# Optimization experiments

Measured on AMD Instinct MI355X. Metric: run time of the kernel, lower is better.

The kernel has to match this reference:

```python
import jax, jax.numpy as jnp
import numpy as np

B = 2_000_000
ND = 3

def _skew(v):
    # v: [B,3] -> [B,3,3] skew-symmetric matrix
    z = jnp.zeros_like(v[..., 0])
    r0 = jnp.stack([z, -v[..., 2], v[..., 1]], axis=-1)
    r1 = jnp.stack([v[..., 2], z, -v[..., 0]], axis=-1)
    r2 = jnp.stack([-v[..., 1], v[..., 0], z], axis=-1)
    return jnp.stack([r0, r1, r2], axis=-2)

def _rotmat(v):
    # Closed-form expm of skew(v) (Rodrigues). Mathematically identical to tf.linalg.expm.
    th2 = jnp.sum(v * v, axis=-1)                      # [B]
    th = jnp.sqrt(th2)
    small = th < 1e-6
    th_s = jnp.where(small, 1.0, th)
    th2_s = jnp.where(small, 1.0, th2)
    a = jnp.where(small, 1.0, jnp.sin(th) / th_s)      # sin(t)/t
    b = jnp.where(small, 0.5, (1.0 - jnp.cos(th)) / th2_s)  # (1-cos t)/t^2
    K = _skew(v)                                       # [B,3,3]
    I = jnp.eye(ND, dtype=v.dtype)
    return I + a[:, None, None] * K + b[:, None, None] * jnp.matmul(K, K)

def setup_inputs() -> dict:
    key = jax.random.key(0)
    k1, k2, k3, k4 = jax.random.split(key, 4)
    trans = jax.random.normal(k1, (B, ND), dtype=jnp.float32)
    rotat = jax.random.normal(k2, (B, ND), dtype=jnp.float32)
    scal_dir = jax.random.normal(k3, (B, ND), dtype=jnp.float32)
    scal = jax.random.normal(k4, (B, ND), dtype=jnp.float32)
    return {"trans": trans, "rotat": rotat, "scal_dir": scal_dir, "scal": scal}

def reference(trans, rotat, scal_dir, scal):
    R = _rotmat(rotat)          # [B,3,3] rotation
    U = _rotmat(scal_dir)       # [B,3,3] scaling direction
    D = jnp.exp(scal)           # expm(diag(s)) == diag(exp(s)), [B,3]
    # U @ diag(D) @ U^T, then R @ (.)
    Ut = jnp.swapaxes(U, -1, -2)
    M = jnp.matmul(U, D[:, :, None] * Ut)   # diag(D) @ U^T broadcast as row-scaling
    M = jnp.matmul(R, M)
    return jnp.concatenate([M, trans[:, :, None]], axis=2)  # [B,3,4]
```

## Files before the change

kernel.cpp:

```cpp
#include <hip/hip_runtime.h>
#include <math.h>

#define TPB 256
#define WPW (TPB / 64)
#define NBLOCKS 1024

__device__ __forceinline__ void rodrigues(float v0, float v1, float v2, float R[9]) {
    float th2 = v0 * v0 + v1 * v1 + v2 * v2;
    bool  sm  = th2 < 1e-12f;
    float g   = sm ? 1.0f : th2;
    float inv = rsqrtf(g);
    float th  = g * inv;
    float s   = __sinf(th);
    float c   = __cosf(th);
    float a   = sm ? 1.0f : s * inv;
    float b   = sm ? 0.5f : (1.0f - c) * (inv * inv);
    float cc  = 1.0f - b * th2;
    R[0] = cc + b * v0 * v0;      R[1] = b * v0 * v1 - a * v2;  R[2] = b * v0 * v2 + a * v1;
    R[3] = b * v0 * v1 + a * v2;  R[4] = cc + b * v1 * v1;      R[5] = b * v1 * v2 - a * v0;
    R[6] = b * v0 * v2 - a * v1;  R[7] = b * v1 * v2 + a * v0;  R[8] = cc + b * v2 * v2;
}

__device__ __forceinline__ void load12(const float* __restrict__ trans,
                                       const float* __restrict__ rotat,
                                       const float* __restrict__ sdir,
                                       const float* __restrict__ scal,
                                       int b3, float p[12]) {
    p[0] = trans[b3]; p[1]  = trans[b3+1]; p[2]  = trans[b3+2];
    p[3] = rotat[b3]; p[4]  = rotat[b3+1]; p[5]  = rotat[b3+2];
    p[6] = sdir [b3]; p[7]  = sdir [b3+1]; p[8]  = sdir [b3+2];
    p[9] = scal [b3]; p[10] = scal [b3+1]; p[11] = scal [b3+2];
}

__global__ __launch_bounds__(TPB) void aff_kernel(
    const float* __restrict__ trans,
    const float* __restrict__ rotat,
    const float* __restrict__ sdir,
    const float* __restrict__ scal,
    float4* __restrict__ out,
    int T)
{
    __shared__ float4 s_out[WPW][192];
    const int w   = threadIdx.x >> 6;
    const int l   = threadIdx.x & 63;
    float4* slab  = s_out[w];
    const int wid = blockIdx.x * WPW + w;
    const int W   = gridDim.x * WPW;

    int t = wid;
    if (t >= T) return;

    float p[12];
    load12(trans, rotat, sdir, scal, 3 * ((t << 6) + l), p);

    while (true) {
        float c[12];
#pragma unroll
        for (int i = 0; i < 12; ++i) c[i] = p[i];

        const int tn = t + W;
        if (tn < T) load12(trans, rotat, sdir, scal, 3 * ((tn << 6) + l), p);

        float R[9], U[9];
        rodrigues(c[3], c[4], c[5], R);
        rodrigues(c[6], c[7], c[8], U);
        float d0 = __expf(c[9]);
        float d1 = __expf(c[10]);
        float d2 = __expf(c[11]);

        float Wm[9];
#pragma unroll
        for (int i = 0; i < 3; ++i) {
            Wm[3*i+0] = U[3*i+0] * d0;
            Wm[3*i+1] = U[3*i+1] * d1;
            Wm[3*i+2] = U[3*i+2] * d2;
        }
        float S[9];
#pragma unroll
        for (int i = 0; i < 3; ++i)
#pragma unroll
            for (int j = 0; j < 3; ++j)
                S[3*i+j] = Wm[3*i+0]*U[3*j+0] + Wm[3*i+1]*U[3*j+1] + Wm[3*i+2]*U[3*j+2];
        float M[9];
#pragma unroll
        for (int i = 0; i < 3; ++i)
#pragma unroll
            for (int j = 0; j < 3; ++j)
                M[3*i+j] = R[3*i+0]*S[0+j] + R[3*i+1]*S[3+j] + R[3*i+2]*S[6+j];

        slab[3*l + 0] = make_float4(M[0], M[1], M[2], c[0]);
        slab[3*l + 1] = make_float4(M[3], M[4], M[5], c[1]);
        slab[3*l + 2] = make_float4(M[6], M[7], M[8], c[2]);
        __builtin_amdgcn_wave_barrier();

        const int ob = 192 * t;
#pragma unroll
        for (int k = 0; k < 3; ++k) {
            int idx = (k << 6) + l;
            out[ob + idx] = slab[idx];
        }

        if (tn >= T) break;
        t = tn;
    }
}

extern "C" void kernel_launch(void* const* d_in, const int* in_sizes, int n_in,
                              void* d_out, int out_size, void* d_ws, size_t ws_size,
                              hipStream_t stream) {
    const float* tr = (const float*)d_in[0];
    const float* ro = (const float*)d_in[1];
    const float* sd = (const float*)d_in[2];
    const float* sc = (const float*)d_in[3];
    float4* out = (float4*)d_out;

    int B = in_sizes[0] / 3;
    int T = B >> 6;
    int blocks = NBLOCKS;
    if (blocks * WPW > T) blocks = (T + WPW - 1) / WPW;
    aff_kernel<<<blocks, TPB, 0, stream>>>(tr, ro, sd, sc, out, T);
}
```

Before: 177.5 us.

## Stage inputs through LDS with coalesced float4 loads per wave

Each wave now loads its 64 elements' inputs as contiguous float4 vectors (48 lanes per array) and stages them through a per-wave shared-memory slab, where each lane then reads its own 3 floats. This replaces twelve strided scalar global loads per lane with four wide coalesced loads. The grid also grows from 1024 to 1536 blocks. In exchange there is extra LDS traffic and shared memory, a wave barrier, and 16 idle lanes during the loads.

```diff
diff --git a/kernel.cpp b/kernel.cpp
--- a/kernel.cpp
+++ b/kernel.cpp
@@ -1,9 +1,9 @@
 #include <hip/hip_runtime.h>
 #include <math.h>
 
-#define TPB 256
-#define WPW (TPB / 64)
-#define NBLOCKS 1024
+#define TPB  256
+#define WPB  4
+#define NBLK 1536
 
 __device__ __forceinline__ void rodrigues(float v0, float v1, float v2, float R[9]) {
     float th2 = v0 * v0 + v1 * v1 + v2 * v2;
@@ -21,52 +21,61 @@
     R[6] = b * v0 * v2 - a * v1;  R[7] = b * v1 * v2 + a * v0;  R[8] = cc + b * v2 * v2;
 }
 
-__device__ __forceinline__ void load12(const float* __restrict__ trans,
-                                       const float* __restrict__ rotat,
-                                       const float* __restrict__ sdir,
-                                       const float* __restrict__ scal,
-                                       int b3, float p[12]) {
-    p[0] = trans[b3]; p[1]  = trans[b3+1]; p[2]  = trans[b3+2];
-    p[3] = rotat[b3]; p[4]  = rotat[b3+1]; p[5]  = rotat[b3+2];
-    p[6] = sdir [b3]; p[7]  = sdir [b3+1]; p[8]  = sdir [b3+2];
-    p[9] = scal [b3]; p[10] = scal [b3+1]; p[11] = scal [b3+2];
-}
-
 __global__ __launch_bounds__(TPB) void aff_kernel(
-    const float* __restrict__ trans,
-    const float* __restrict__ rotat,
-    const float* __restrict__ sdir,
-    const float* __restrict__ scal,
+    const float4* __restrict__ tr4,
+    const float4* __restrict__ ro4,
+    const float4* __restrict__ sd4,
+    const float4* __restrict__ sc4,
     float4* __restrict__ out,
     int T)
 {
-    __shared__ float4 s_out[WPW][192];
-    const int w   = threadIdx.x >> 6;
-    const int l   = threadIdx.x & 63;
-    float4* slab  = s_out[w];
-    const int wid = blockIdx.x * WPW + w;
-    const int W   = gridDim.x * WPW;
+    __shared__ float4 s_in [WPB][4 * 48];
+    __shared__ float4 s_out[WPB][192];
 
+    const int w = threadIdx.x >> 6;
+    const int l = threadIdx.x & 63;
+    float4* islab = s_in[w];
+    const float* ifl = (const float*)islab;
+    float4* oslab = s_out[w];
+
+    const int wid = blockIdx.x * WPB + w;
+    const int W   = gridDim.x * WPB;
     int t = wid;
     if (t >= T) return;
 
-    float p[12];
-    load12(trans, rotat, sdir, scal, 3 * ((t << 6) + l), p);
+    float4 p0, p1, p2, p3;
+    if (l < 48) {
+        int g = t * 48 + l;
+        p0 = tr4[g]; p1 = ro4[g]; p2 = sd4[g]; p3 = sc4[g];
+    }
 
     while (true) {
-        float c[12];
-#pragma unroll
-        for (int i = 0; i < 12; ++i) c[i] = p[i];
+        float4 c0 = p0, c1 = p1, c2 = p2, c3 = p3;
+        const int tn = t + W;
+        if (tn < T && l < 48) {
+            int g = tn * 48 + l;
+            p0 = tr4[g]; p1 = ro4[g]; p2 = sd4[g]; p3 = sc4[g];
+        }
 
-        const int tn = t + W;
-        if (tn < T) load12(trans, rotat, sdir, scal, 3 * ((tn << 6) + l), p);
+        if (l < 48) {
+            islab[0 * 48 + l] = c0;
+            islab[1 * 48 + l] = c1;
+            islab[2 * 48 + l] = c2;
+            islab[3 * 48 + l] = c3;
+        }
+        __builtin_amdgcn_wave_barrier();
+
+        float t0 = ifl[0 * 192 + 3 * l], t1 = ifl[0 * 192 + 3 * l + 1], t2 = ifl[0 * 192 + 3 * l + 2];
+        float r0 = ifl[1 * 192 + 3 * l], r1 = ifl[1 * 192 + 3 * l + 1], r2 = ifl[1 * 192 + 3 * l + 2];
+        float u0 = ifl[2 * 192 + 3 * l], u1 = ifl[2 * 192 + 3 * l + 1], u2 = ifl[2 * 192 + 3 * l + 2];
+        float s0 = ifl[3 * 192 + 3 * l], s1 = ifl[3 * 192 + 3 * l + 1], s2 = ifl[3 * 192 + 3 * l + 2];
 
         float R[9], U[9];
-        rodrigues(c[3], c[4], c[5], R);
-        rodrigues(c[6], c[7], c[8], U);
-        float d0 = __expf(c[9]);
-        float d1 = __expf(c[10]);
-        float d2 = __expf(c[11]);
+        rodrigues(r0, r1, r2, R);
+        rodrigues(u0, u1, u2, U);
+        float d0 = __expf(s0);
+        float d1 = __expf(s1);
+        float d2 = __expf(s2);
 
         float Wm[9];
 #pragma unroll
@@ -88,16 +97,16 @@
             for (int j = 0; j < 3; ++j)
                 M[3*i+j] = R[3*i+0]*S[0+j] + R[3*i+1]*S[3+j] + R[3*i+2]*S[6+j];
 
-        slab[3*l + 0] = make_float4(M[0], M[1], M[2], c[0]);
-        slab[3*l + 1] = make_float4(M[3], M[4], M[5], c[1]);
-        slab[3*l + 2] = make_float4(M[6], M[7], M[8], c[2]);
+        oslab[3*l + 0] = make_float4(M[0], M[1], M[2], t0);
+        oslab[3*l + 1] = make_float4(M[3], M[4], M[5], t1);
+        oslab[3*l + 2] = make_float4(M[6], M[7], M[8], t2);
         __builtin_amdgcn_wave_barrier();
 
         const int ob = 192 * t;
 #pragma unroll
         for (int k = 0; k < 3; ++k) {
             int idx = (k << 6) + l;
-            out[ob + idx] = slab[idx];
+            out[ob + idx] = oslab[idx];
         }
 
         if (tn >= T) break;
@@ -108,15 +117,15 @@
 extern "C" void kernel_launch(void* const* d_in, const int* in_sizes, int n_in,
                               void* d_out, int out_size, void* d_ws, size_t ws_size,
                               hipStream_t stream) {
-    const float* tr = (const float*)d_in[0];
-    const float* ro = (const float*)d_in[1];
-    const float* sd = (const float*)d_in[2];
-    const float* sc = (const float*)d_in[3];
+    const float4* tr = (const float4*)d_in[0];
+    const float4* ro = (const float4*)d_in[1];
+    const float4* sd = (const float4*)d_in[2];
+    const float4* sc = (const float4*)d_in[3];
     float4* out = (float4*)d_out;
 
     int B = in_sizes[0] / 3;
     int T = B >> 6;
-    int blocks = NBLOCKS;
-    if (blocks * WPW > T) blocks = (T + WPW - 1) / WPW;
+    int blocks = NBLK;
+    if (blocks * WPB > T) blocks = (T + WPB - 1) / WPB;
     aff_kernel<<<blocks, TPB, 0, stream>>>(tr, ro, sd, sc, out, T);
 }
```

Measured after the change: 177.8 us. About the same (+0.2%).
